# Performance work log

Hardware: AMD Instinct MI355X
Metric: run time of the kernel (lower is better)

Reference implementation:

```python
import jax, jax.numpy as jnp
import numpy as np

EMBED = 1024
HEADS = 16
HEAD_DIM = EMBED // HEADS
T = 1024
B = 2
TEMP = 1.0
EPS = 1e-20


def setup_inputs() -> dict:
    key = jax.random.key(0)
    ks = jax.random.split(key, 8)
    s = 0.02  # xavier-ish init scale
    return {
        "g": jax.random.normal(ks[0], (T, B, EMBED), dtype=jnp.float32),
        "h": jax.random.normal(ks[1], (T, B, EMBED), dtype=jnp.float32),
        "g_in_w": jax.random.normal(ks[2], (3 * EMBED, EMBED), dtype=jnp.float32) * s,
        "g_in_b": jnp.zeros((3 * EMBED,), dtype=jnp.float32),
        "h_in_w": jax.random.normal(ks[3], (2 * EMBED, EMBED), dtype=jnp.float32) * s,
        "h_in_b": jnp.zeros((2 * EMBED,), dtype=jnp.float32),
        "g_out_w": jax.random.normal(ks[4], (EMBED, EMBED), dtype=jnp.float32) * s,
        "g_out_b": jnp.zeros((EMBED,), dtype=jnp.float32),
        "h_out_w": jax.random.normal(ks[5], (EMBED, EMBED), dtype=jnp.float32) * s,
        "h_out_b": jnp.zeros((EMBED,), dtype=jnp.float32),
    }


def reference(g, h, g_in_w, g_in_b, h_in_w, h_in_b, g_out_w, g_out_b, h_out_w, h_out_b):
    Tt, Bb, E = g.shape
    H, d = HEADS, HEAD_DIM

    # fused qkv projection on g stream, kv on h stream (F.linear: x @ W^T + b)
    q, gk, gv = jnp.split(g @ g_in_w.T + g_in_b, 3, axis=-1)
    hk, hv = jnp.split(h @ h_in_w.T + h_in_b, 2, axis=-1)
    q = q * (d ** -0.5)

    def to_heads(x):  # [T,B,E] -> [B,H,T,d]
        return x.reshape(Tt, Bb, H, d).transpose(1, 2, 0, 3)

    q, gk, gv, hk, hv = map(to_heads, (q, gk, gv, hk, hv))

    # dual-stream attention scores
    g_scores = jnp.einsum("bhtd,bhsd->bhts", q, gk)
    h_scores = jnp.einsum("bhtd,bhsd->bhts", q, hk)

    g_p = jax.nn.softmax(g_scores, axis=-1)
    h_p = jax.nn.softmax(h_scores, axis=-1)

    # gumbel-softmax sample of h_scores (mode='gumbel', temperature=TEMP)
    u = jax.random.uniform(jax.random.key(42), h_scores.shape, dtype=h_scores.dtype)
    noise = -jnp.log(-jnp.log(u + EPS) + EPS)
    sample = jax.nn.softmax((jax.nn.log_softmax(h_scores, axis=-1) + noise) / TEMP, axis=-1)

    g_attn = jnp.einsum("bhts,bhsd->bhtd", g_p, gv)
    h_attn = jnp.einsum("bhts,bhsd->bhtd", sample, hv)

    def merge(x):  # [B,H,T,d] -> [T,B,E]
        return x.transpose(2, 0, 1, 3).reshape(Tt, Bb, E)

    g_out = merge(g_attn) @ g_out_w.T + g_out_b
    h_out = merge(h_attn) @ h_out_w.T + h_out_b
    return g_out, h_out
```

## Files before the change

kernel.cpp:

```cpp
#include <hip/hip_runtime.h>
#include <stdint.h>

#define T_SEQ 1024

typedef __attribute__((ext_vector_type(8))) short short8;
typedef __attribute__((ext_vector_type(4))) float f32x4;
typedef __attribute__((ext_vector_type(4))) unsigned short ushort4v;
typedef __attribute__((ext_vector_type(8))) unsigned short ushort8v;

__device__ __forceinline__ unsigned short f2bf(float f) {
  union { float f; uint32_t u; } v; v.f = f;
  return (unsigned short)((v.u + 0x7fffu + ((v.u >> 16) & 1u)) >> 16);
}
__device__ __forceinline__ float bf2f(unsigned short u) {
  union { uint32_t u; float f; } v; v.u = ((uint32_t)u) << 16;
  return v.f;
}

__device__ __forceinline__ void gl2lds16(const unsigned short* g, unsigned short* l) {
  __builtin_amdgcn_global_load_lds(
      (const __attribute__((address_space(1))) void*)g,
      (__attribute__((address_space(3))) void*)l, 16, 0, 0);
}

__device__ __forceinline__ uint32_t tf_bits(uint32_t flat) {
  const uint32_t ks1 = 42u;
  const uint32_t ks2 = 0x1BD11BDAu ^ 42u;
  uint32_t x0 = 0u;
  uint32_t x1 = flat + ks1;
#define TFR(r) { x0 += x1; x1 = (x1 << (r)) | (x1 >> (32 - (r))); x1 ^= x0; }
  TFR(13) TFR(15) TFR(26) TFR(6)
  x0 += ks1; x1 += ks2 + 1u;
  TFR(17) TFR(29) TFR(16) TFR(24)
  x0 += ks2; x1 += 2u;
  TFR(13) TFR(15) TFR(26) TFR(6)
  x1 += ks1 + 3u;
  TFR(17) TFR(29) TFR(16) TFR(24)
  x0 += ks1; x1 += ks2 + 4u;
  TFR(13) TFR(15) TFR(26) TFR(6)
  x0 += ks2; x1 += 5u;
#undef TFR
  return x0 ^ x1;
}

__device__ __forceinline__ float gumbel_noise(uint32_t flat) {
  const uint32_t bits = tf_bits(flat);
  const float u = __uint_as_float((bits >> 9) | 0x3f800000u) - 1.0f;
  return -__logf(-__logf(u + 1e-20f) + 1e-20f);
}

__global__ __launch_bounds__(256) void convert_pre(
    const float* __restrict__ g, const float* __restrict__ h,
    const float* __restrict__ wgi_f, const float* __restrict__ whi_f,
    const float* __restrict__ wgo_f, const float* __restrict__ who_f,
    unsigned short* __restrict__ gbf, unsigned short* __restrict__ hbf,
    unsigned short* __restrict__ wgi, unsigned short* __restrict__ whi,
    unsigned short* __restrict__ wgo, unsigned short* __restrict__ who)
{
  const int64_t Q_SPLIT = 1048576;
  const int64_t Q_TOTAL = Q_SPLIT + 1835008;
  for (int64_t qd = (int64_t)blockIdx.x * 256 + threadIdx.x; qd < Q_TOTAL;
       qd += (int64_t)gridDim.x * 256) {
    if (qd < Q_SPLIT) {
      const int which = qd >= 524288;
      const int64_t e = (qd - (which ? 524288 : 0)) * 4;
      const float4 v = *(const float4*)((which ? h : g) + e);
      ushort4v u = {f2bf(v.x), f2bf(v.y), f2bf(v.z), f2bf(v.w)};
      *(ushort4v*)((which ? hbf : gbf) + e) = u;
    } else {
      int64_t off = qd - Q_SPLIT;
      const float* src; unsigned short* dst;
      if (off < 786432)                 { src = wgi_f; dst = wgi; }
      else if (off < 1310720)           { off -= 786432;  src = whi_f; dst = whi; }
      else if (off < 1572864)           { off -= 1310720; src = wgo_f; dst = wgo; }
      else                              { off -= 1572864; src = who_f; dst = who; }
      const int64_t e = off * 4;
      const float4 v = *(const float4*)(src + e);
      ushort4v u = {f2bf(v.x), f2bf(v.y), f2bf(v.z), f2bf(v.w)};
      *(ushort4v*)(dst + e) = u;
    }
  }
}

template<int TM, bool BF16OUT>
__device__ __forceinline__ void gemm_plain_core(
    const unsigned short* __restrict__ Ab, const unsigned short* __restrict__ Wb,
    const float* __restrict__ bias, int N, int K, int m0, int n0,
    int scale_limit, void* Cout, unsigned short* sA, unsigned short* sW)
{
  const int tid = threadIdx.x;
  const int w = tid >> 6;
  const int lane = tid & 63;
  const int txl = lane & 15, q = lane >> 4;
  const int wr = (w >> 1) * (TM * 16);
  const int wc = (w & 1) << 6;
  const int lr = lane >> 3, lu = lane & 7;
  const int rx7 = txl & 7;

  const unsigned short* Asrc = Ab + (size_t)(m0 + w * 8 * TM + lr) * K + ((lu ^ lr) << 3);
  const unsigned short* Wsrc = Wb + (size_t)(n0 + w * 32 + lr) * K + ((lu ^ lr) << 3);
  unsigned short* sAd = sA + (w * 8 * TM) * 64;
  unsigned short* sWd = sW + (w * 32) * 64;

  f32x4 acc[TM][4];
#pragma unroll
  for (int i = 0; i < TM; i++)
#pragma unroll
    for (int j = 0; j < 4; j++) acc[i][j] = (f32x4){0.f, 0.f, 0.f, 0.f};

  for (int k0 = 0; k0 < K; k0 += 64) {
    __syncthreads();
#pragma unroll
    for (int i = 0; i < TM; i++)
      gl2lds16(Asrc + (size_t)(8 * i) * K + k0, sAd + (8 * i) * 64);
#pragma unroll
    for (int i = 0; i < 4; i++)
      gl2lds16(Wsrc + (size_t)(8 * i) * K + k0, sWd + (8 * i) * 64);
    __syncthreads();
#pragma unroll
    for (int kk = 0; kk < 2; kk++) {
      const int uoff = ((4 * kk + q) ^ rx7) << 3;
      short8 af[TM], wf[4];
#pragma unroll
      for (int i = 0; i < TM; i++)
        af[i] = *(const short8*)&sA[(wr + 16 * i + txl) * 64 + uoff];
#pragma unroll
      for (int j = 0; j < 4; j++)
        wf[j] = *(const short8*)&sW[(wc + 16 * j + txl) * 64 + uoff];
#pragma unroll
      for (int i = 0; i < TM; i++)
#pragma unroll
        for (int j = 0; j < 4; j++)
          acc[i][j] = __builtin_amdgcn_mfma_f32_16x16x32_bf16(af[i], wf[j], acc[i][j], 0, 0, 0);
    }
  }

#pragma unroll
  for (int j = 0; j < 4; j++) {
    const int col = n0 + wc + 16 * j + txl;
    const float bj = bias[col];
    const float sc = (col < scale_limit) ? 0.125f : 1.0f;
#pragma unroll
    for (int i = 0; i < TM; i++) {
      const int rbase = m0 + wr + 16 * i + 4 * q;
#pragma unroll
      for (int r = 0; r < 4; r++) {
        const float v = (acc[i][j][r] + bj) * sc;
        if (BF16OUT) ((unsigned short*)Cout)[(size_t)(rbase + r) * N + col] = f2bf(v);
        else         ((float*)Cout)[(size_t)(rbase + r) * N + col] = v;
      }
    }
  }
}

__global__ __launch_bounds__(256, 4) void gemm_inproj(
    const unsigned short* __restrict__ gbf, const unsigned short* __restrict__ wgi,
    const float* __restrict__ bgi,
    const unsigned short* __restrict__ hbf, const unsigned short* __restrict__ whi,
    const float* __restrict__ bhi,
    unsigned short* __restrict__ qkv, unsigned short* __restrict__ hkv)
{
  __shared__ __align__(16) unsigned short sm[16384];
  const int bx = blockIdx.x;
  const int m0 = blockIdx.y * 128;
  if (bx < 24)
    gemm_plain_core<4, true>(gbf, wgi, bgi, 3072, 1024, m0, bx * 128, 1024,
                             qkv, sm, sm + 8192);
  else
    gemm_plain_core<4, true>(hbf, whi, bhi, 2048, 1024, m0, (bx - 24) * 128, 0,
                             hkv, sm, sm + 8192);
}

__global__ __launch_bounds__(256, 2) void gemm_outproj(
    const unsigned short* __restrict__ attnb,
    const unsigned short* __restrict__ wgo, const float* __restrict__ bgo,
    const unsigned short* __restrict__ who, const float* __restrict__ bho,
    float* __restrict__ out)
{
  __shared__ __align__(16) unsigned short sm[12288];
  const int m0 = blockIdx.y * 64;
  const unsigned short* Wp = (m0 < 2048) ? wgo : who;
  const float* bp = (m0 < 2048) ? bgo : bho;
  gemm_plain_core<2, false>(attnb, Wp, bp, 1024, 1024, m0, blockIdx.x * 128, 0,
                            out, sm, sm + 4096);
}

__global__ __launch_bounds__(256, 4) void attn_mfma(
    const unsigned short* __restrict__ qkv, const unsigned short* __restrict__ hkv,
    float* __restrict__ Opart, float* __restrict__ lpart)
{
  __shared__ __align__(16) unsigned short smem[18432];
  unsigned short* KV = smem;
  unsigned short* PC = smem + 9216;
  unsigned short* QS = smem + 9216;

  const int tid = threadIdx.x;
  const int w = tid >> 6;
  const int lane = tid & 63;
  const int txl = lane & 15, q = lane >> 4;
  const int t0 = blockIdx.x * 64;
  const int bh = blockIdx.y;
  const int z = blockIdx.z;
  const int b = bh >> 4;
  const int head = bh & 15;
  const int hoff = head * 64;
  const int sr = tid >> 2;
  const int sc = (tid & 3) << 4;

  {
    const size_t gq = ((size_t)(t0 + sr) * 2 + b) * 3072 + hoff + sc;
    *(ushort8v*)&QS[sr * 72 + sc]     = *(const ushort8v*)&qkv[gq];
    *(ushort8v*)&QS[sr * 72 + sc + 8] = *(const ushort8v*)&qkv[gq + 8];
  }
  __syncthreads();
  const short8 aq0 = *(const short8*)&QS[(16 * w + txl) * 72 + 8 * q];
  const short8 aq1 = *(const short8*)&QS[(16 * w + txl) * 72 + 32 + 8 * q];

  f32x4 Og[4], Oh[4];
  float l_g[4], l_h[4];
#pragma unroll
  for (int i = 0; i < 4; i++) {
    Og[i] = (f32x4){0.f, 0.f, 0.f, 0.f};
    Oh[i] = (f32x4){0.f, 0.f, 0.f, 0.f};
    l_g[i] = 0.f; l_h[i] = 0.f;
  }

  unsigned short* pcg = PC + (w * 2 + 0) * 1152;
  unsigned short* pch = PC + (w * 2 + 1) * 1152;

  const int s_begin = z * (T_SEQ / 2);
  const int s_end = s_begin + (T_SEQ / 2);
  for (int s0 = s_begin; s0 < s_end; s0 += 64) {
    __syncthreads();
    {
      const size_t grow = (size_t)(s0 + sr) * 2 + b;
      const ushort8v kg0 = *(const ushort8v*)&qkv[grow * 3072 + 1024 + hoff + sc];
      const ushort8v kg1 = *(const ushort8v*)&qkv[grow * 3072 + 1024 + hoff + sc + 8];
      const ushort8v kh0 = *(const ushort8v*)&hkv[grow * 2048 + hoff + sc];
      const ushort8v kh1 = *(const ushort8v*)&hkv[grow * 2048 + hoff + sc + 8];
      *(ushort8v*)&KV[sr * 72 + sc]            = kg0;
      *(ushort8v*)&KV[sr * 72 + sc + 8]        = kg1;
      *(ushort8v*)&KV[4608 + sr * 72 + sc]     = kh0;
      *(ushort8v*)&KV[4608 + sr * 72 + sc + 8] = kh1;
    }
    __syncthreads();

    f32x4 Sg[4], Sh[4];
    const f32x4 zz = (f32x4){0.f, 0.f, 0.f, 0.f};
#pragma unroll
    for (int nt = 0; nt < 4; nt++) {
      const int srw = (16 * nt + txl) * 72;
      const short8 bg0 = *(const short8*)&KV[srw + 8 * q];
      const short8 bg1 = *(const short8*)&KV[srw + 32 + 8 * q];
      const short8 bh0 = *(const short8*)&KV[4608 + srw + 8 * q];
      const short8 bh1 = *(const short8*)&KV[4608 + srw + 32 + 8 * q];
      f32x4 ag = __builtin_amdgcn_mfma_f32_16x16x32_bf16(aq0, bg0, zz, 0, 0, 0);
      ag = __builtin_amdgcn_mfma_f32_16x16x32_bf16(aq1, bg1, ag, 0, 0, 0);
      f32x4 ah = __builtin_amdgcn_mfma_f32_16x16x32_bf16(aq0, bh0, zz, 0, 0, 0);
      ah = __builtin_amdgcn_mfma_f32_16x16x32_bf16(aq1, bh1, ah, 0, 0, 0);
      Sg[nt] = ag; Sh[nt] = ah;
    }

#pragma unroll
    for (int nt = 0; nt < 4; nt++)
#pragma unroll
      for (int r = 0; r < 4; r++) {
        const uint32_t trow = (uint32_t)(t0 + 16 * w + 4 * q + r);
        const uint32_t scol_ = (uint32_t)(s0 + 16 * nt + txl);
        Sh[nt][r] += gumbel_noise(((uint32_t)bh << 20) | (trow << 10) | scol_);
      }

#pragma unroll
    for (int nt = 0; nt < 4; nt++) {
      float eg[4], eh[4];
#pragma unroll
      for (int r = 0; r < 4; r++) {
        eg[r] = __expf(Sg[nt][r]); l_g[r] += eg[r];
        eh[r] = __expf(Sh[nt][r]); l_h[r] += eh[r];
      }
      const int sbase = (16 * nt + txl) * 18 + 4 * q;
      *(uint32_t*)&pcg[sbase]     = (uint32_t)f2bf(eg[0]) | ((uint32_t)f2bf(eg[1]) << 16);
      *(uint32_t*)&pcg[sbase + 2] = (uint32_t)f2bf(eg[2]) | ((uint32_t)f2bf(eg[3]) << 16);
      *(uint32_t*)&pch[sbase]     = (uint32_t)f2bf(eh[0]) | ((uint32_t)f2bf(eh[1]) << 16);
      *(uint32_t*)&pch[sbase + 2] = (uint32_t)f2bf(eh[2]) | ((uint32_t)f2bf(eh[3]) << 16);
    }

    __syncthreads();
    {
      const int dd = tid >> 2;
      const int sseg = (tid & 3) * 16;
      ushort8v vg[2], vh[2];
#pragma unroll
      for (int p = 0; p < 2; p++)
#pragma unroll
        for (int m = 0; m < 8; m++) {
          const int s = sseg + 8 * p + m;
          const size_t grow = (size_t)(s0 + s) * 2 + b;
          vg[p][m] = qkv[grow * 3072 + 2048 + hoff + dd];
          vh[p][m] = hkv[grow * 2048 + 1024 + hoff + dd];
        }
#pragma unroll
      for (int p = 0; p < 2; p++) {
        *(ushort8v*)&KV[dd * 72 + sseg + 8 * p]        = vg[p];
        *(ushort8v*)&KV[4608 + dd * 72 + sseg + 8 * p] = vh[p];
      }
    }
    __syncthreads();

#pragma unroll
    for (int c = 0; c < 2; c++) {
      short8 apg, aph;
#pragma unroll
      for (int j = 0; j < 8; j++) {
        apg[j] = (short)pcg[(32 * c + 8 * q + j) * 18 + txl];
        aph[j] = (short)pch[(32 * c + 8 * q + j) * 18 + txl];
      }
#pragma unroll
      for (int nt = 0; nt < 4; nt++) {
        const int drow = (16 * nt + txl) * 72;
        const short8 bvg = *(const short8*)&KV[drow + 32 * c + 8 * q];
        const short8 bvh = *(const short8*)&KV[4608 + drow + 32 * c + 8 * q];
        Og[nt] = __builtin_amdgcn_mfma_f32_16x16x32_bf16(apg, bvg, Og[nt], 0, 0, 0);
        Oh[nt] = __builtin_amdgcn_mfma_f32_16x16x32_bf16(aph, bvh, Oh[nt], 0, 0, 0);
      }
    }
  }

  float* opg = Opart + ((size_t)(z * 2 + 0) * 2048) * 1024;
  float* oph = Opart + ((size_t)(z * 2 + 1) * 2048) * 1024;
  float* lpg = lpart + (size_t)(z * 2 + 0) * 2048 * 16;
  float* lph = lpart + (size_t)(z * 2 + 1) * 2048 * 16;
#pragma unroll
  for (int r = 0; r < 4; r++) {
    float lg = l_g[r], lh = l_h[r];
    lg += __shfl_xor(lg, 1); lg += __shfl_xor(lg, 2);
    lg += __shfl_xor(lg, 4); lg += __shfl_xor(lg, 8);
    lh += __shfl_xor(lh, 1); lh += __shfl_xor(lh, 2);
    lh += __shfl_xor(lh, 4); lh += __shfl_xor(lh, 8);
    const int row = (t0 + 16 * w + 4 * q + r) * 2 + b;
    if (txl == 0) {
      lpg[row * 16 + head] = lg;
      lph[row * 16 + head] = lh;
    }
    const size_t base = (size_t)row * 1024 + hoff;
#pragma unroll
    for (int nt = 0; nt < 4; nt++) {
      opg[base + 16 * nt + txl] = Og[nt][r];
      oph[base + 16 * nt + txl] = Oh[nt][r];
    }
  }
}

__global__ __launch_bounds__(256) void merge_attn(
    const float* __restrict__ Opart, const float* __restrict__ lpart,
    unsigned short* __restrict__ attnb)
{
  const int idx = blockIdx.x * 256 + threadIdx.x;
  const int st = idx >> 19;
  const int i = idx & 0x7FFFF;
  const int row = i >> 8;
  const int colq = i & 255;
  const int head = colq >> 4;
  const float4 o0 = *(const float4*)&Opart[((size_t)(0 + st) * 2048 + row) * 1024 + colq * 4];
  const float4 o1 = *(const float4*)&Opart[((size_t)(2 + st) * 2048 + row) * 1024 + colq * 4];
  const float l0 = lpart[(size_t)(0 + st) * 32768 + row * 16 + head];
  const float l1 = lpart[(size_t)(2 + st) * 32768 + row * 16 + head];
  const float inv = 1.0f / (l0 + l1);
  ushort4v u = {f2bf((o0.x + o1.x) * inv), f2bf((o0.y + o1.y) * inv),
                f2bf((o0.z + o1.z) * inv), f2bf((o0.w + o1.w) * inv)};
  *(ushort4v*)&attnb[((size_t)st * 2048 + row) * 1024 + colq * 4] = u;
}

extern "C" void kernel_launch(void* const* d_in, const int* in_sizes, int n_in,
                              void* d_out, int out_size, void* d_ws, size_t ws_size,
                              hipStream_t stream) {
  const float* g       = (const float*)d_in[0];
  const float* h       = (const float*)d_in[1];
  const float* g_in_w  = (const float*)d_in[2];
  const float* g_in_b  = (const float*)d_in[3];
  const float* h_in_w  = (const float*)d_in[4];
  const float* h_in_b  = (const float*)d_in[5];
  const float* g_out_w = (const float*)d_in[6];
  const float* g_out_b = (const float*)d_in[7];
  const float* h_out_w = (const float*)d_in[8];
  const float* h_out_b = (const float*)d_in[9];
  float* out = (float*)d_out;

  unsigned short* ws = (unsigned short*)d_ws;
  unsigned short* qkv   = ws;
  unsigned short* hkv   = qkv + (size_t)2048*3072;
  unsigned short* attnb = hkv + (size_t)2048*2048;
  unsigned short* wgo   = attnb + (size_t)4096*1024;
  unsigned short* who   = wgo + (size_t)1024*1024;
  unsigned short* scratch = who + (size_t)1024*1024;
  unsigned short* gbf = scratch;
  unsigned short* hbf = gbf + (size_t)2048*1024;
  unsigned short* wgi = hbf + (size_t)2048*1024;
  unsigned short* whi = wgi + (size_t)3072*1024;
  float* Opart = (float*)scratch;
  float* lpart = Opart + (size_t)4*2048*1024;

  convert_pre<<<1024, 256, 0, stream>>>(g, h, g_in_w, h_in_w, g_out_w, h_out_w,
                                        gbf, hbf, wgi, whi, wgo, who);
  gemm_inproj<<<dim3(40, 16), 256, 0, stream>>>(
      gbf, wgi, g_in_b, hbf, whi, h_in_b, qkv, hkv);
  attn_mfma<<<dim3(T_SEQ / 64, 32, 2), 256, 0, stream>>>(qkv, hkv, Opart, lpart);
  merge_attn<<<4096, 256, 0, stream>>>(Opart, lpart, attnb);
  gemm_outproj<<<dim3(8, 64), 256, 0, stream>>>(
      attnb, wgo, g_out_b, who, h_out_b, out);
}
```

Baseline: 282.4 us.

## Pre-transpose V and stream K/V tiles via direct global-to-LDS swizzled loads

Adds a kernel that transposes the g and h value blocks into [b, d, t] layout. The attention kernel can then load V tiles with 16-byte direct global-to-LDS transfers instead of strided 2-byte scalar gathers. K tiles also move to direct global-to-LDS loads, using an XOR-swizzled unpadded LDS layout to avoid bank conflicts, which shrinks shared memory. Gumbel noise is computed while the K loads are in flight, and the P fragments are read before the V barrier. The cost is an extra kernel launch plus a round trip to global memory for the transposed V.

```diff
diff --git a/kernel.cpp b/kernel.cpp
--- a/kernel.cpp
+++ b/kernel.cpp
@@ -185,19 +185,57 @@
                             out, sm, sm + 4096);
 }
 
+__global__ __launch_bounds__(256) void transpose_v(
+    const unsigned short* __restrict__ qkv, const unsigned short* __restrict__ hkv,
+    unsigned short* __restrict__ vTg, unsigned short* __restrict__ vTh)
+{
+  __shared__ __align__(16) unsigned short sm[64 * 72];
+  const int tid = threadIdx.x;
+  const int t0 = blockIdx.x * 64;
+  const int d0 = blockIdx.y * 64;
+  const int zb = blockIdx.z;
+  const int b = zb & 1;
+  const int strm = zb >> 1;
+  const unsigned short* src = strm ? hkv : qkv;
+  const int srcoff = strm ? 1024 : 2048;
+  const int sstride = strm ? 2048 : 3072;
+  unsigned short* dst = strm ? vTh : vTg;
+
+  const int r = tid >> 2, cs = (tid & 3) << 4;
+  {
+    const size_t gsrc = (size_t)((t0 + r) * 2 + b) * sstride + srcoff + d0 + cs;
+    *(ushort8v*)&sm[r * 72 + cs]     = *(const ushort8v*)&src[gsrc];
+    *(ushort8v*)&sm[r * 72 + cs + 8] = *(const ushort8v*)&src[gsrc + 8];
+  }
+  __syncthreads();
+  const int dr = tid >> 2, ts = (tid & 3) << 4;
+  ushort8v o0, o1;
+#pragma unroll
+  for (int m = 0; m < 8; m++) o0[m] = sm[(ts + m) * 72 + dr];
+#pragma unroll
+  for (int m = 0; m < 8; m++) o1[m] = sm[(ts + 8 + m) * 72 + dr];
+  const size_t gdst = (size_t)b * 1048576 + (size_t)(d0 + dr) * 1024 + t0 + ts;
+  *(ushort8v*)&dst[gdst]     = o0;
+  *(ushort8v*)&dst[gdst + 8] = o1;
+}
+
 __global__ __launch_bounds__(256, 4) void attn_mfma(
     const unsigned short* __restrict__ qkv, const unsigned short* __restrict__ hkv,
+    const unsigned short* __restrict__ vTg, const unsigned short* __restrict__ vTh,
     float* __restrict__ Opart, float* __restrict__ lpart)
 {
-  __shared__ __align__(16) unsigned short smem[18432];
+  __shared__ __align__(16) unsigned short smem[17408];
   unsigned short* KV = smem;
-  unsigned short* PC = smem + 9216;
-  unsigned short* QS = smem + 9216;
+  unsigned short* PC = smem + 8192;
+  unsigned short* QS = smem + 8192;
 
   const int tid = threadIdx.x;
   const int w = tid >> 6;
   const int lane = tid & 63;
   const int txl = lane & 15, q = lane >> 4;
+  const int rx7 = txl & 7;
+  const int lr = lane >> 3, lu = lane & 7;
+  const int su = (lu ^ lr) << 3;
   const int t0 = blockIdx.x * 64;
   const int bh = blockIdx.y;
   const int z = blockIdx.z;
@@ -232,28 +270,35 @@
   const int s_end = s_begin + (T_SEQ / 2);
   for (int s0 = s_begin; s0 < s_end; s0 += 64) {
     __syncthreads();
-    {
-      const size_t grow = (size_t)(s0 + sr) * 2 + b;
-      const ushort8v kg0 = *(const ushort8v*)&qkv[grow * 3072 + 1024 + hoff + sc];
-      const ushort8v kg1 = *(const ushort8v*)&qkv[grow * 3072 + 1024 + hoff + sc + 8];
-      const ushort8v kh0 = *(const ushort8v*)&hkv[grow * 2048 + hoff + sc];
-      const ushort8v kh1 = *(const ushort8v*)&hkv[grow * 2048 + hoff + sc + 8];
-      *(ushort8v*)&KV[sr * 72 + sc]            = kg0;
-      *(ushort8v*)&KV[sr * 72 + sc + 8]        = kg1;
-      *(ushort8v*)&KV[4608 + sr * 72 + sc]     = kh0;
-      *(ushort8v*)&KV[4608 + sr * 72 + sc + 8] = kh1;
-    }
+#pragma unroll
+    for (int t = 0; t < 2; t++) {
+      const int srow = w * 16 + t * 8 + lr;
+      const size_t grow = (size_t)(s0 + srow) * 2 + b;
+      gl2lds16(&qkv[grow * 3072 + 1024 + hoff + su], &KV[(w * 16 + t * 8) * 64]);
+      gl2lds16(&hkv[grow * 2048 +        hoff + su], &KV[4096 + (w * 16 + t * 8) * 64]);
+    }
+    float ng[4][4];
+#pragma unroll
+    for (int nt = 0; nt < 4; nt++)
+#pragma unroll
+      for (int r = 0; r < 4; r++) {
+        const uint32_t trow = (uint32_t)(t0 + 16 * w + 4 * q + r);
+        const uint32_t scol_ = (uint32_t)(s0 + 16 * nt + txl);
+        ng[nt][r] = gumbel_noise(((uint32_t)bh << 20) | (trow << 10) | scol_);
+      }
     __syncthreads();
 
     f32x4 Sg[4], Sh[4];
     const f32x4 zz = (f32x4){0.f, 0.f, 0.f, 0.f};
 #pragma unroll
     for (int nt = 0; nt < 4; nt++) {
-      const int srw = (16 * nt + txl) * 72;
-      const short8 bg0 = *(const short8*)&KV[srw + 8 * q];
-      const short8 bg1 = *(const short8*)&KV[srw + 32 + 8 * q];
-      const short8 bh0 = *(const short8*)&KV[4608 + srw + 8 * q];
-      const short8 bh1 = *(const short8*)&KV[4608 + srw + 32 + 8 * q];
+      const int srw = (16 * nt + txl) * 64;
+      const int u0 = (q ^ rx7) << 3;
+      const int u1 = ((4 + q) ^ rx7) << 3;
+      const short8 bg0 = *(const short8*)&KV[srw + u0];
+      const short8 bg1 = *(const short8*)&KV[srw + u1];
+      const short8 bh0 = *(const short8*)&KV[4096 + srw + u0];
+      const short8 bh1 = *(const short8*)&KV[4096 + srw + u1];
       f32x4 ag = __builtin_amdgcn_mfma_f32_16x16x32_bf16(aq0, bg0, zz, 0, 0, 0);
       ag = __builtin_amdgcn_mfma_f32_16x16x32_bf16(aq1, bg1, ag, 0, 0, 0);
       f32x4 ah = __builtin_amdgcn_mfma_f32_16x16x32_bf16(aq0, bh0, zz, 0, 0, 0);
@@ -262,21 +307,12 @@
     }
 
 #pragma unroll
-    for (int nt = 0; nt < 4; nt++)
-#pragma unroll
-      for (int r = 0; r < 4; r++) {
-        const uint32_t trow = (uint32_t)(t0 + 16 * w + 4 * q + r);
-        const uint32_t scol_ = (uint32_t)(s0 + 16 * nt + txl);
-        Sh[nt][r] += gumbel_noise(((uint32_t)bh << 20) | (trow << 10) | scol_);
-      }
-
-#pragma unroll
     for (int nt = 0; nt < 4; nt++) {
       float eg[4], eh[4];
 #pragma unroll
       for (int r = 0; r < 4; r++) {
-        eg[r] = __expf(Sg[nt][r]); l_g[r] += eg[r];
-        eh[r] = __expf(Sh[nt][r]); l_h[r] += eh[r];
+        eg[r] = __expf(Sg[nt][r]);            l_g[r] += eg[r];
+        eh[r] = __expf(Sh[nt][r] + ng[nt][r]); l_h[r] += eh[r];
       }
       const int sbase = (16 * nt + txl) * 18 + 4 * q;
       *(uint32_t*)&pcg[sbase]     = (uint32_t)f2bf(eg[0]) | ((uint32_t)f2bf(eg[1]) << 16);
@@ -286,42 +322,33 @@
     }
 
     __syncthreads();
-    {
-      const int dd = tid >> 2;
-      const int sseg = (tid & 3) * 16;
-      ushort8v vg[2], vh[2];
-#pragma unroll
-      for (int p = 0; p < 2; p++)
-#pragma unroll
-        for (int m = 0; m < 8; m++) {
-          const int s = sseg + 8 * p + m;
-          const size_t grow = (size_t)(s0 + s) * 2 + b;
-          vg[p][m] = qkv[grow * 3072 + 2048 + hoff + dd];
-          vh[p][m] = hkv[grow * 2048 + 1024 + hoff + dd];
-        }
-#pragma unroll
-      for (int p = 0; p < 2; p++) {
-        *(ushort8v*)&KV[dd * 72 + sseg + 8 * p]        = vg[p];
-        *(ushort8v*)&KV[4608 + dd * 72 + sseg + 8 * p] = vh[p];
+#pragma unroll
+    for (int t = 0; t < 2; t++) {
+      const int drow = w * 16 + t * 8 + lr;
+      const size_t gv = (size_t)b * 1048576 + (size_t)(hoff + drow) * 1024 + s0 + su;
+      gl2lds16(&vTg[gv], &KV[(w * 16 + t * 8) * 64]);
+      gl2lds16(&vTh[gv], &KV[4096 + (w * 16 + t * 8) * 64]);
+    }
+    short8 apg[2], aph[2];
+#pragma unroll
+    for (int c = 0; c < 2; c++)
+#pragma unroll
+      for (int j = 0; j < 8; j++) {
+        apg[c][j] = (short)pcg[(32 * c + 8 * q + j) * 18 + txl];
+        aph[c][j] = (short)pch[(32 * c + 8 * q + j) * 18 + txl];
       }
-    }
     __syncthreads();
 
 #pragma unroll
     for (int c = 0; c < 2; c++) {
-      short8 apg, aph;
-#pragma unroll
-      for (int j = 0; j < 8; j++) {
-        apg[j] = (short)pcg[(32 * c + 8 * q + j) * 18 + txl];
-        aph[j] = (short)pch[(32 * c + 8 * q + j) * 18 + txl];
-      }
 #pragma unroll
       for (int nt = 0; nt < 4; nt++) {
-        const int drow = (16 * nt + txl) * 72;
-        const short8 bvg = *(const short8*)&KV[drow + 32 * c + 8 * q];
-        const short8 bvh = *(const short8*)&KV[4608 + drow + 32 * c + 8 * q];
-        Og[nt] = __builtin_amdgcn_mfma_f32_16x16x32_bf16(apg, bvg, Og[nt], 0, 0, 0);
-        Oh[nt] = __builtin_amdgcn_mfma_f32_16x16x32_bf16(aph, bvh, Oh[nt], 0, 0, 0);
+        const int drw = (16 * nt + txl) * 64;
+        const int uv = (((4 * c + q) ^ rx7)) << 3;
+        const short8 bvg = *(const short8*)&KV[drw + uv];
+        const short8 bvh = *(const short8*)&KV[4096 + drw + uv];
+        Og[nt] = __builtin_amdgcn_mfma_f32_16x16x32_bf16(apg[c], bvg, Og[nt], 0, 0, 0);
+        Oh[nt] = __builtin_amdgcn_mfma_f32_16x16x32_bf16(aph[c], bvh, Oh[nt], 0, 0, 0);
       }
     }
   }
@@ -399,12 +426,15 @@
   unsigned short* whi = wgi + (size_t)3072*1024;
   float* Opart = (float*)scratch;
   float* lpart = Opart + (size_t)4*2048*1024;
+  unsigned short* vTg = (unsigned short*)(lpart + (size_t)4*2048*16);
+  unsigned short* vTh = vTg + (size_t)2*1024*1024;
 
   convert_pre<<<1024, 256, 0, stream>>>(g, h, g_in_w, h_in_w, g_out_w, h_out_w,
                                         gbf, hbf, wgi, whi, wgo, who);
   gemm_inproj<<<dim3(40, 16), 256, 0, stream>>>(
       gbf, wgi, g_in_b, hbf, whi, h_in_b, qkv, hkv);
-  attn_mfma<<<dim3(T_SEQ / 64, 32, 2), 256, 0, stream>>>(qkv, hkv, Opart, lpart);
+  transpose_v<<<dim3(16, 16, 4), 256, 0, stream>>>(qkv, hkv, vTg, vTh);
+  attn_mfma<<<dim3(T_SEQ / 64, 32, 2), 256, 0, stream>>>(qkv, hkv, vTg, vTh, Opart, lpart);
   merge_attn<<<4096, 256, 0, stream>>>(Opart, lpart, attnb);
   gemm_outproj<<<dim3(8, 64), 256, 0, stream>>>(
       attnb, wgo, g_out_b, who, h_out_b, out);
```

After: 278.1 us. No clear change (-1.5%).
